# Kernel optimization log

Measured on AMD Instinct MI355X. Metric: run time of the kernel, lower is better.

The kernel has to match this reference:

```python
import jax, jax.numpy as jnp
import numpy as np

NEG_INF = -1e30


def setup_inputs() -> dict:
    key = jax.random.key(0)
    k1, k2, k3 = jax.random.split(key, 3)
    B, H, HKV, S, D = 2, 16, 4, 2048, 128
    q = jax.random.normal(k1, (B, H, S, D), dtype=jnp.float32)
    k = jax.random.normal(k2, (B, HKV, S, D), dtype=jnp.float32)
    v = jax.random.normal(k3, (B, HKV, S, D), dtype=jnp.float32)
    return {"q": q, "k": k, "v": v}


def reference(q, k, v):
    # Flash attention math (exact, non-tiled reference): causal + sliding-window
    # masked softmax(QK^T * scale) V with GQA head grouping.
    B, H, M, D = q.shape
    _, HKV, N, _ = k.shape
    G = H // HKV  # num_kv_groups
    W = 512       # sliding window size
    scale = 1.0 / jnp.sqrt(jnp.float32(D))

    qg = q.reshape(B, HKV, G, M, D)
    # scores: [B, HKV, G, M, N]
    scores = jnp.einsum("bkgmd,bknd->bkgmn", qg, k) * scale

    i = jnp.arange(M)[:, None]
    j = jnp.arange(N)[None, :]
    # causal: j <= i ; sliding window: only last W keys visible (i - j < W)
    keep = (j <= i) & ((i - j) < W)
    scores = jnp.where(keep[None, None, None], scores, NEG_INF)

    p = jax.nn.softmax(scores.astype(jnp.float32), axis=-1).astype(q.dtype)
    out = jnp.einsum("bkgmn,bknd->bkgmd", p, v)
    return out.reshape(B, H, M, D)
```

## Files before the change

kernel.cpp:

```cpp
#include <hip/hip_runtime.h>
#include <hip/hip_bf16.h>
#include <stdint.h>

#define SEQ 2048
#define HD  128
#define WIN 512
#define NH  16
#define NKV 4
#define BATCH 2

typedef __attribute__((ext_vector_type(8))) short bf16x8;
typedef __attribute__((ext_vector_type(4))) short bf16x4;
typedef __attribute__((ext_vector_type(4))) float f32x4;
typedef __attribute__((ext_vector_type(4))) uint32_t u32x4;
typedef __attribute__((ext_vector_type(2))) uint32_t u32x2;

#define EXP2(x) __builtin_amdgcn_exp2f(x)

#define KSTR 136
#define VSTR 72

__device__ __forceinline__ uint32_t pk2(float a, float b) {
    __hip_bfloat162 h = __float22bfloat162_rn(make_float2(a, b));
    return *reinterpret_cast<uint32_t*>(&h);
}

__device__ __forceinline__ f32x4 mfma16(bf16x4 a, bf16x4 b, f32x4 c) {
#if __has_builtin(__builtin_amdgcn_mfma_f32_16x16x16bf16_1k)
    return __builtin_amdgcn_mfma_f32_16x16x16bf16_1k(a, b, c, 0, 0, 0);
#else
    asm volatile("v_mfma_f32_16x16x16_bf16 %0, %1, %2, %0\n\ts_nop 7\n\ts_nop 7"
                 : "+v"(c) : "v"(a), "v"(b));
    return c;
#endif
}

__global__ __launch_bounds__(256) __attribute__((amdgpu_waves_per_eu(2, 2)))
void fa_mfma(
    const float* __restrict__ q,
    const float* __restrict__ k,
    const float* __restrict__ v,
    float* __restrict__ out)
{
    const int tid  = threadIdx.x;
    const int wave = tid >> 6;
    const int lane = tid & 63;
    const int l4   = lane >> 4;
    const int l15  = lane & 15;

    const int bh   = blockIdx.x >> 4;
    const int qblk = blockIdx.x & 15;
    const int q0   = qblk << 7;
    const int hkv  = (bh & (NH - 1)) >> 2;
    const int b    = bh >> 4;

    const int i0   = q0 + wave * 32;

    __shared__ __align__(16) uint16_t lds_k[2][64 * KSTR];
    __shared__ __align__(16) uint16_t lds_vt[2][HD * VSTR];

    const float scale2 = 0.08838834764831845f * 1.4426950408889634f;

    const size_t qbase  = (size_t)bh * SEQ * HD;
    const size_t kvbase = (size_t)(b * NKV + hkv) * SEQ * HD;

    bf16x8 qf[2][4];
    #pragma unroll
    for (int nt = 0; nt < 2; ++nt) {
        const float* qr = q + qbase + (size_t)(i0 + nt * 16 + l15) * HD;
        #pragma unroll
        for (int ks = 0; ks < 4; ++ks) {
            const float4* g = reinterpret_cast<const float4*>(qr + ks * 32 + l4 * 8);
            float4 a = g[0], bq = g[1];
            u32x4 t;
            t.x = pk2(a.x * scale2, a.y * scale2);
            t.y = pk2(a.z * scale2, a.w * scale2);
            t.z = pk2(bq.x * scale2, bq.y * scale2);
            t.w = pk2(bq.z * scale2, bq.w * scale2);
            qf[nt][ks] = __builtin_bit_cast(bf16x8, t);
        }
    }

    f32x4 O[2][8];
    #pragma unroll
    for (int a1 = 0; a1 < 2; ++a1)
        #pragma unroll
        for (int a2 = 0; a2 < 8; ++a2) O[a1][a2] = (f32x4){0.f, 0.f, 0.f, 0.f};
    float mrow[2] = {-1e30f, -1e30f};
    float lrow[2] = {0.f, 0.f};

    const int kt_lo_blk = (q0 >= 512) ? ((q0 - 511) >> 6) : 0;
    const int kt_hi_blk = (q0 + 127) >> 6;
    const int lo_w = (i0 >= 512) ? ((i0 - 511) >> 6) : 0;
    const int hi_w = (i0 + 31) >> 6;

    const int vdg = tid & 31;
    const int vkg = tid >> 5;
    float4 rKa[4], rKb[4], rV[8];

    auto prefetch_k = [&](int kt) {
        const float* kp = k + kvbase + (size_t)kt * 64 * HD;
        #pragma unroll
        for (int it = 0; it < 4; ++it) {
            int flat8 = tid + it * 256, key = flat8 >> 4, ch = flat8 & 15;
            const float4* g = reinterpret_cast<const float4*>(kp + key * HD + ch * 8);
            rKa[it] = g[0]; rKb[it] = g[1];
        }
    };
    auto prefetch_v = [&](int kt) {
        const float* vp = v + kvbase + (size_t)kt * 64 * HD;
        #pragma unroll
        for (int r = 0; r < 8; ++r)
            rV[r] = *reinterpret_cast<const float4*>(vp + (vkg * 8 + r) * HD + vdg * 4);
    };

    auto pack_k = [&](int pb) {
        #pragma unroll
        for (int it = 0; it < 4; ++it) {
            int flat8 = tid + it * 256, key = flat8 >> 4, ch = flat8 & 15;
            uint4 wv;
            wv.x = pk2(rKa[it].x, rKa[it].y);  wv.y = pk2(rKa[it].z, rKa[it].w);
            wv.z = pk2(rKb[it].x, rKb[it].y);  wv.w = pk2(rKb[it].z, rKb[it].w);
            *reinterpret_cast<uint4*>(&lds_k[pb][key * KSTR + ch * 8]) = wv;
        }
    };
    auto pack_v = [&](int pb) {
        const float* rvf = reinterpret_cast<const float*>(rV);
        #pragma unroll
        for (int i = 0; i < 4; ++i) {
            uint4 wv;
            wv.x = pk2(rvf[0 * 4 + i], rvf[1 * 4 + i]);
            wv.y = pk2(rvf[2 * 4 + i], rvf[3 * 4 + i]);
            wv.z = pk2(rvf[4 * 4 + i], rvf[5 * 4 + i]);
            wv.w = pk2(rvf[6 * 4 + i], rvf[7 * 4 + i]);
            *reinterpret_cast<uint4*>(&lds_vt[pb][(vdg * 4 + i) * VSTR + vkg * 8]) = wv;
        }
    };

    prefetch_k(kt_lo_blk);
    prefetch_v(kt_lo_blk);
    pack_k(0);
    pack_v(0);
    __syncthreads();

    int par = 0;
    for (int kt = kt_lo_blk; kt <= kt_hi_blk; ++kt) {
        const bool more = (kt < kt_hi_blk);
        if (more) prefetch_k(kt + 1);

        if (kt >= lo_w && kt <= hi_w) {
            f32x4 sf[4][2];
            #pragma unroll
            for (int mt = 0; mt < 4; ++mt) {
                #pragma unroll
                for (int nt = 0; nt < 2; ++nt) sf[mt][nt] = (f32x4){0.f, 0.f, 0.f, 0.f};
                #pragma unroll
                for (int ks = 0; ks < 4; ++ks) {
                    bf16x8 af = *reinterpret_cast<const bf16x8*>(
                        &lds_k[par][(mt * 16 + l15) * KSTR + ks * 32 + l4 * 8]);
                    #pragma unroll
                    for (int nt = 0; nt < 2; ++nt)
                        sf[mt][nt] = __builtin_amdgcn_mfma_f32_16x16x32_bf16(
                            af, qf[nt][ks], sf[mt][nt], 0, 0, 0);
                }
            }
            if (more) { pack_k(par ^ 1); prefetch_v(kt + 1); }
            const bool needmask = (kt == hi_w) || (kt == lo_w && i0 > 511);
            if (needmask) {
                #pragma unroll
                for (int mt = 0; mt < 4; ++mt) {
                    int jb = kt * 64 + mt * 16 + l4 * 4;
                    #pragma unroll
                    for (int nt = 0; nt < 2; ++nt) {
                        int iq = i0 + nt * 16 + l15;
                        #pragma unroll
                        for (int r = 0; r < 4; ++r) {
                            int j = jb + r;
                            if (!((j <= iq) && (iq - j < WIN))) sf[mt][nt][r] = -1e30f;
                        }
                    }
                }
            }
            float tm[2];
            #pragma unroll
            for (int nt = 0; nt < 2; ++nt) {
                float a0 = fmaxf(fmaxf(sf[0][nt][0], sf[0][nt][1]),
                                 fmaxf(sf[0][nt][2], sf[0][nt][3]));
                float a1 = fmaxf(fmaxf(sf[1][nt][0], sf[1][nt][1]),
                                 fmaxf(sf[1][nt][2], sf[1][nt][3]));
                float a2 = fmaxf(fmaxf(sf[2][nt][0], sf[2][nt][1]),
                                 fmaxf(sf[2][nt][2], sf[2][nt][3]));
                float a3 = fmaxf(fmaxf(sf[3][nt][0], sf[3][nt][1]),
                                 fmaxf(sf[3][nt][2], sf[3][nt][3]));
                float t = fmaxf(fmaxf(a0, a1), fmaxf(a2, a3));
                t = fmaxf(t, __shfl_xor(t, 16, 64));
                t = fmaxf(t, __shfl_xor(t, 32, 64));
                tm[nt] = t;
            }
            const bool defer = __all(tm[0] <= mrow[0] + 8.0f) &&
                               __all(tm[1] <= mrow[1] + 8.0f);
            if (!defer) {
                float alpha[2];
                #pragma unroll
                for (int nt = 0; nt < 2; ++nt) {
                    float mn = fmaxf(mrow[nt], tm[nt]);
                    alpha[nt] = EXP2(mrow[nt] - mn);
                    mrow[nt] = mn;
                    lrow[nt] *= alpha[nt];
                }
                #pragma unroll
                for (int mt = 0; mt < 2; ++mt) {
                    #pragma unroll
                    for (int r = 0; r < 4; ++r) {
                        float ar = __shfl(alpha[mt], l4 * 4 + r, 64);
                        #pragma unroll
                        for (int nt = 0; nt < 8; ++nt) O[mt][nt][r] *= ar;
                    }
                }
            }
            bf16x4 pfrag[4][2];
            #pragma unroll
            for (int nt = 0; nt < 2; ++nt) {
                float me = fmaxf(mrow[nt], -1e20f);
                float s[4];
                #pragma unroll
                for (int mt = 0; mt < 4; ++mt) {
                    float p0 = EXP2(sf[mt][nt][0] - me);
                    float p1 = EXP2(sf[mt][nt][1] - me);
                    float p2 = EXP2(sf[mt][nt][2] - me);
                    float p3 = EXP2(sf[mt][nt][3] - me);
                    u32x2 t;
                    t.x = pk2(p0, p1);
                    t.y = pk2(p2, p3);
                    pfrag[mt][nt] = __builtin_bit_cast(bf16x4, t);
                    s[mt] = (p0 + p1) + (p2 + p3);
                }
                float ts = (s[0] + s[1]) + (s[2] + s[3]);
                ts += __shfl_xor(ts, 16, 64);
                ts += __shfl_xor(ts, 32, 64);
                lrow[nt] += ts;
            }
            if (more) pack_v(par ^ 1);
            #pragma unroll
            for (int mt = 0; mt < 4; ++mt) {
                #pragma unroll
                for (int nt = 0; nt < 8; ++nt) {
                    bf16x4 vf = *reinterpret_cast<const bf16x4*>(
                        &lds_vt[par][(nt * 16 + l15) * VSTR + mt * 16 + l4 * 4]);
                    O[0][nt] = mfma16(pfrag[mt][0], vf, O[0][nt]);
                    O[1][nt] = mfma16(pfrag[mt][1], vf, O[1][nt]);
                }
            }
        } else {
            if (more) { prefetch_v(kt + 1); pack_k(par ^ 1); pack_v(par ^ 1); }
        }
        __syncthreads();
        par ^= 1;
    }

    #pragma unroll
    for (int mt = 0; mt < 2; ++mt) {
        float inv = 1.0f / lrow[mt];
        #pragma unroll
        for (int r = 0; r < 4; ++r) {
            float li = __shfl(inv, l4 * 4 + r, 64);
            int row = i0 + mt * 16 + l4 * 4 + r;
            float* orow = out + qbase + (size_t)row * HD;
            #pragma unroll
            for (int nt = 0; nt < 8; ++nt)
                orow[nt * 16 + l15] = O[mt][nt][r] * li;
        }
    }
}

extern "C" void kernel_launch(void* const* d_in, const int* in_sizes, int n_in,
                              void* d_out, int out_size, void* d_ws, size_t ws_size,
                              hipStream_t stream) {
    const float* q = (const float*)d_in[0];
    const float* k = (const float*)d_in[1];
    const float* v = (const float*)d_in[2];
    float* out     = (float*)d_out;

    hipLaunchKernelGGL(fa_mfma, dim3(BATCH * NH * (SEQ / 128)), dim3(256), 0, stream,
                       q, k, v, out);
}
```

Baseline: 139.3 us.

## Use 8 waves of 16 query rows each and 16x16x32 MFMA for PV

Doubles the block to 512 threads so each wave owns 16 query rows instead of 32, cutting per-wave accumulator and score registers and raising waves per EU. The PV product switches from 16x16x16 MFMA to 16x16x32 MFMA by concatenating pairs of P and V fragments. s_setprio is added around the MFMA phases. Each wave now reuses each K/V LDS fragment for fewer rows, so LDS read traffic per FLOP rises, and the synchronization is shared by more waves.

```diff
diff --git a/kernel.cpp b/kernel.cpp
--- a/kernel.cpp
+++ b/kernel.cpp
@@ -25,17 +25,7 @@
     return *reinterpret_cast<uint32_t*>(&h);
 }
 
-__device__ __forceinline__ f32x4 mfma16(bf16x4 a, bf16x4 b, f32x4 c) {
-#if __has_builtin(__builtin_amdgcn_mfma_f32_16x16x16bf16_1k)
-    return __builtin_amdgcn_mfma_f32_16x16x16bf16_1k(a, b, c, 0, 0, 0);
-#else
-    asm volatile("v_mfma_f32_16x16x16_bf16 %0, %1, %2, %0\n\ts_nop 7\n\ts_nop 7"
-                 : "+v"(c) : "v"(a), "v"(b));
-    return c;
-#endif
-}
-
-__global__ __launch_bounds__(256) __attribute__((amdgpu_waves_per_eu(2, 2)))
+__global__ __launch_bounds__(512) __attribute__((amdgpu_waves_per_eu(4, 4)))
 void fa_mfma(
     const float* __restrict__ q,
     const float* __restrict__ k,
@@ -54,7 +44,7 @@
     const int hkv  = (bh & (NH - 1)) >> 2;
     const int b    = bh >> 4;
 
-    const int i0   = q0 + wave * 32;
+    const int i0   = q0 + wave * 16;
 
     __shared__ __align__(16) uint16_t lds_k[2][64 * KSTR];
     __shared__ __align__(16) uint16_t lds_vt[2][HD * VSTR];
@@ -64,10 +54,9 @@
     const size_t qbase  = (size_t)bh * SEQ * HD;
     const size_t kvbase = (size_t)(b * NKV + hkv) * SEQ * HD;
 
-    bf16x8 qf[2][4];
-    #pragma unroll
-    for (int nt = 0; nt < 2; ++nt) {
-        const float* qr = q + qbase + (size_t)(i0 + nt * 16 + l15) * HD;
+    bf16x8 qf[4];
+    {
+        const float* qr = q + qbase + (size_t)(i0 + l15) * HD;
         #pragma unroll
         for (int ks = 0; ks < 4; ++ks) {
             const float4* g = reinterpret_cast<const float4*>(qr + ks * 32 + l4 * 8);
@@ -77,32 +66,30 @@
             t.y = pk2(a.z * scale2, a.w * scale2);
             t.z = pk2(bq.x * scale2, bq.y * scale2);
             t.w = pk2(bq.z * scale2, bq.w * scale2);
-            qf[nt][ks] = __builtin_bit_cast(bf16x8, t);
+            qf[ks] = __builtin_bit_cast(bf16x8, t);
         }
     }
 
-    f32x4 O[2][8];
+    f32x4 O[8];
     #pragma unroll
-    for (int a1 = 0; a1 < 2; ++a1)
-        #pragma unroll
-        for (int a2 = 0; a2 < 8; ++a2) O[a1][a2] = (f32x4){0.f, 0.f, 0.f, 0.f};
-    float mrow[2] = {-1e30f, -1e30f};
-    float lrow[2] = {0.f, 0.f};
+    for (int a2 = 0; a2 < 8; ++a2) O[a2] = (f32x4){0.f, 0.f, 0.f, 0.f};
+    float mrow = -1e30f;
+    float lrow = 0.f;
 
     const int kt_lo_blk = (q0 >= 512) ? ((q0 - 511) >> 6) : 0;
     const int kt_hi_blk = (q0 + 127) >> 6;
     const int lo_w = (i0 >= 512) ? ((i0 - 511) >> 6) : 0;
-    const int hi_w = (i0 + 31) >> 6;
+    const int hi_w = (i0 + 15) >> 6;
 
     const int vdg = tid & 31;
     const int vkg = tid >> 5;
-    float4 rKa[4], rKb[4], rV[8];
+    float4 rKa[2], rKb[2], rV[4];
 
     auto prefetch_k = [&](int kt) {
         const float* kp = k + kvbase + (size_t)kt * 64 * HD;
         #pragma unroll
-        for (int it = 0; it < 4; ++it) {
-            int flat8 = tid + it * 256, key = flat8 >> 4, ch = flat8 & 15;
+        for (int it = 0; it < 2; ++it) {
+            int flat8 = tid + it * 512, key = flat8 >> 4, ch = flat8 & 15;
             const float4* g = reinterpret_cast<const float4*>(kp + key * HD + ch * 8);
             rKa[it] = g[0]; rKb[it] = g[1];
         }
@@ -110,14 +97,14 @@
     auto prefetch_v = [&](int kt) {
         const float* vp = v + kvbase + (size_t)kt * 64 * HD;
         #pragma unroll
-        for (int r = 0; r < 8; ++r)
-            rV[r] = *reinterpret_cast<const float4*>(vp + (vkg * 8 + r) * HD + vdg * 4);
+        for (int r = 0; r < 4; ++r)
+            rV[r] = *reinterpret_cast<const float4*>(vp + (vkg * 4 + r) * HD + vdg * 4);
     };
 
     auto pack_k = [&](int pb) {
         #pragma unroll
-        for (int it = 0; it < 4; ++it) {
-            int flat8 = tid + it * 256, key = flat8 >> 4, ch = flat8 & 15;
+        for (int it = 0; it < 2; ++it) {
+            int flat8 = tid + it * 512, key = flat8 >> 4, ch = flat8 & 15;
             uint4 wv;
             wv.x = pk2(rKa[it].x, rKa[it].y);  wv.y = pk2(rKa[it].z, rKa[it].w);
             wv.z = pk2(rKb[it].x, rKb[it].y);  wv.w = pk2(rKb[it].z, rKb[it].w);
@@ -128,12 +115,10 @@
         const float* rvf = reinterpret_cast<const float*>(rV);
         #pragma unroll
         for (int i = 0; i < 4; ++i) {
-            uint4 wv;
+            u32x2 wv;
             wv.x = pk2(rvf[0 * 4 + i], rvf[1 * 4 + i]);
             wv.y = pk2(rvf[2 * 4 + i], rvf[3 * 4 + i]);
-            wv.z = pk2(rvf[4 * 4 + i], rvf[5 * 4 + i]);
-            wv.w = pk2(rvf[6 * 4 + i], rvf[7 * 4 + i]);
-            *reinterpret_cast<uint4*>(&lds_vt[pb][(vdg * 4 + i) * VSTR + vkg * 8]) = wv;
+            *reinterpret_cast<u32x2*>(&lds_vt[pb][(vdg * 4 + i) * VSTR + vkg * 4]) = wv;
         }
     };
 
@@ -149,108 +134,92 @@
         if (more) prefetch_k(kt + 1);
 
         if (kt >= lo_w && kt <= hi_w) {
-            f32x4 sf[4][2];
+            f32x4 sf[4];
+            #pragma unroll
+            for (int mt = 0; mt < 4; ++mt) sf[mt] = (f32x4){0.f, 0.f, 0.f, 0.f};
+            __builtin_amdgcn_s_setprio(1);
             #pragma unroll
             for (int mt = 0; mt < 4; ++mt) {
-                #pragma unroll
-                for (int nt = 0; nt < 2; ++nt) sf[mt][nt] = (f32x4){0.f, 0.f, 0.f, 0.f};
                 #pragma unroll
                 for (int ks = 0; ks < 4; ++ks) {
                     bf16x8 af = *reinterpret_cast<const bf16x8*>(
                         &lds_k[par][(mt * 16 + l15) * KSTR + ks * 32 + l4 * 8]);
-                    #pragma unroll
-                    for (int nt = 0; nt < 2; ++nt)
-                        sf[mt][nt] = __builtin_amdgcn_mfma_f32_16x16x32_bf16(
-                            af, qf[nt][ks], sf[mt][nt], 0, 0, 0);
-                }
-            }
+                    sf[mt] = __builtin_amdgcn_mfma_f32_16x16x32_bf16(
+                        af, qf[ks], sf[mt], 0, 0, 0);
+                }
+            }
+            __builtin_amdgcn_s_setprio(0);
             if (more) { pack_k(par ^ 1); prefetch_v(kt + 1); }
             const bool needmask = (kt == hi_w) || (kt == lo_w && i0 > 511);
             if (needmask) {
+                const int iq = i0 + l15;
                 #pragma unroll
                 for (int mt = 0; mt < 4; ++mt) {
                     int jb = kt * 64 + mt * 16 + l4 * 4;
                     #pragma unroll
-                    for (int nt = 0; nt < 2; ++nt) {
-                        int iq = i0 + nt * 16 + l15;
-                        #pragma unroll
-                        for (int r = 0; r < 4; ++r) {
-                            int j = jb + r;
-                            if (!((j <= iq) && (iq - j < WIN))) sf[mt][nt][r] = -1e30f;
-                        }
+                    for (int r = 0; r < 4; ++r) {
+                        int j = jb + r;
+                        if (!((j <= iq) && (iq - j < WIN))) sf[mt][r] = -1e30f;
                     }
                 }
             }
-            float tm[2];
-            #pragma unroll
-            for (int nt = 0; nt < 2; ++nt) {
-                float a0 = fmaxf(fmaxf(sf[0][nt][0], sf[0][nt][1]),
-                                 fmaxf(sf[0][nt][2], sf[0][nt][3]));
-                float a1 = fmaxf(fmaxf(sf[1][nt][0], sf[1][nt][1]),
-                                 fmaxf(sf[1][nt][2], sf[1][nt][3]));
-                float a2 = fmaxf(fmaxf(sf[2][nt][0], sf[2][nt][1]),
-                                 fmaxf(sf[2][nt][2], sf[2][nt][3]));
-                float a3 = fmaxf(fmaxf(sf[3][nt][0], sf[3][nt][1]),
-                                 fmaxf(sf[3][nt][2], sf[3][nt][3]));
-                float t = fmaxf(fmaxf(a0, a1), fmaxf(a2, a3));
-                t = fmaxf(t, __shfl_xor(t, 16, 64));
-                t = fmaxf(t, __shfl_xor(t, 32, 64));
-                tm[nt] = t;
-            }
-            const bool defer = __all(tm[0] <= mrow[0] + 8.0f) &&
-                               __all(tm[1] <= mrow[1] + 8.0f);
+            float a0 = fmaxf(fmaxf(sf[0][0], sf[0][1]), fmaxf(sf[0][2], sf[0][3]));
+            float a1 = fmaxf(fmaxf(sf[1][0], sf[1][1]), fmaxf(sf[1][2], sf[1][3]));
+            float a2 = fmaxf(fmaxf(sf[2][0], sf[2][1]), fmaxf(sf[2][2], sf[2][3]));
+            float a3 = fmaxf(fmaxf(sf[3][0], sf[3][1]), fmaxf(sf[3][2], sf[3][3]));
+            float tm = fmaxf(fmaxf(a0, a1), fmaxf(a2, a3));
+            tm = fmaxf(tm, __shfl_xor(tm, 16, 64));
+            tm = fmaxf(tm, __shfl_xor(tm, 32, 64));
+            const bool defer = __all(tm <= mrow + 8.0f);
             if (!defer) {
-                float alpha[2];
-                #pragma unroll
-                for (int nt = 0; nt < 2; ++nt) {
-                    float mn = fmaxf(mrow[nt], tm[nt]);
-                    alpha[nt] = EXP2(mrow[nt] - mn);
-                    mrow[nt] = mn;
-                    lrow[nt] *= alpha[nt];
-                }
-                #pragma unroll
-                for (int mt = 0; mt < 2; ++mt) {
+                float mn = fmaxf(mrow, tm);
+                float alpha = EXP2(mrow - mn);
+                mrow = mn;
+                lrow *= alpha;
+                #pragma unroll
+                for (int r = 0; r < 4; ++r) {
+                    float ar = __shfl(alpha, l4 * 4 + r, 64);
                     #pragma unroll
-                    for (int r = 0; r < 4; ++r) {
-                        float ar = __shfl(alpha[mt], l4 * 4 + r, 64);
-                        #pragma unroll
-                        for (int nt = 0; nt < 8; ++nt) O[mt][nt][r] *= ar;
-                    }
-                }
-            }
-            bf16x4 pfrag[4][2];
-            #pragma unroll
-            for (int nt = 0; nt < 2; ++nt) {
-                float me = fmaxf(mrow[nt], -1e20f);
+                    for (int nt = 0; nt < 8; ++nt) O[nt][r] *= ar;
+                }
+            }
+            bf16x4 pfrag[4];
+            {
+                float me = fmaxf(mrow, -1e20f);
                 float s[4];
                 #pragma unroll
                 for (int mt = 0; mt < 4; ++mt) {
-                    float p0 = EXP2(sf[mt][nt][0] - me);
-                    float p1 = EXP2(sf[mt][nt][1] - me);
-                    float p2 = EXP2(sf[mt][nt][2] - me);
-                    float p3 = EXP2(sf[mt][nt][3] - me);
+                    float p0 = EXP2(sf[mt][0] - me);
+                    float p1 = EXP2(sf[mt][1] - me);
+                    float p2 = EXP2(sf[mt][2] - me);
+                    float p3 = EXP2(sf[mt][3] - me);
                     u32x2 t;
                     t.x = pk2(p0, p1);
                     t.y = pk2(p2, p3);
-                    pfrag[mt][nt] = __builtin_bit_cast(bf16x4, t);
+                    pfrag[mt] = __builtin_bit_cast(bf16x4, t);
                     s[mt] = (p0 + p1) + (p2 + p3);
                 }
                 float ts = (s[0] + s[1]) + (s[2] + s[3]);
                 ts += __shfl_xor(ts, 16, 64);
                 ts += __shfl_xor(ts, 32, 64);
-                lrow[nt] += ts;
+                lrow += ts;
             }
             if (more) pack_v(par ^ 1);
-            #pragma unroll
-            for (int mt = 0; mt < 4; ++mt) {
+            __builtin_amdgcn_s_setprio(1);
+            #pragma unroll
+            for (int s = 0; s < 2; ++s) {
+                bf16x8 pa = __builtin_shufflevector(pfrag[2 * s], pfrag[2 * s + 1],
+                                                    0, 1, 2, 3, 4, 5, 6, 7);
                 #pragma unroll
                 for (int nt = 0; nt < 8; ++nt) {
-                    bf16x4 vf = *reinterpret_cast<const bf16x4*>(
-                        &lds_vt[par][(nt * 16 + l15) * VSTR + mt * 16 + l4 * 4]);
-                    O[0][nt] = mfma16(pfrag[mt][0], vf, O[0][nt]);
-                    O[1][nt] = mfma16(pfrag[mt][1], vf, O[1][nt]);
-                }
-            }
+                    const uint16_t* vrow = &lds_vt[par][(nt * 16 + l15) * VSTR];
+                    bf16x4 v0 = *reinterpret_cast<const bf16x4*>(vrow + s * 32 + l4 * 4);
+                    bf16x4 v1 = *reinterpret_cast<const bf16x4*>(vrow + s * 32 + 16 + l4 * 4);
+                    bf16x8 vf = __builtin_shufflevector(v0, v1, 0, 1, 2, 3, 4, 5, 6, 7);
+                    O[nt] = __builtin_amdgcn_mfma_f32_16x16x32_bf16(pa, vf, O[nt], 0, 0, 0);
+                }
+            }
+            __builtin_amdgcn_s_setprio(0);
         } else {
             if (more) { prefetch_v(kt + 1); pack_k(par ^ 1); pack_v(par ^ 1); }
         }
@@ -258,17 +227,16 @@
         par ^= 1;
     }
 
-    #pragma unroll
-    for (int mt = 0; mt < 2; ++mt) {
-        float inv = 1.0f / lrow[mt];
+    {
+        float inv = 1.0f / lrow;
         #pragma unroll
         for (int r = 0; r < 4; ++r) {
             float li = __shfl(inv, l4 * 4 + r, 64);
-            int row = i0 + mt * 16 + l4 * 4 + r;
+            int row = i0 + l4 * 4 + r;
             float* orow = out + qbase + (size_t)row * HD;
             #pragma unroll
             for (int nt = 0; nt < 8; ++nt)
-                orow[nt * 16 + l15] = O[mt][nt][r] * li;
+                orow[nt * 16 + l15] = O[nt][r] * li;
         }
     }
 }
@@ -281,6 +249,6 @@
     const float* v = (const float*)d_in[2];
     float* out     = (float*)d_out;
 
-    hipLaunchKernelGGL(fa_mfma, dim3(BATCH * NH * (SEQ / 128)), dim3(256), 0, stream,
+    hipLaunchKernelGGL(fa_mfma, dim3(BATCH * NH * (SEQ / 128)), dim3(512), 0, stream,
                        q, k, v, out);
 }
```

Measured after the change: 157.7 us. 13.3% more time.
